# Kernel optimization log

Hardware: AMD Instinct MI355X
Metric: run time of the kernel (lower is better)

## Reference

```python
import jax, jax.numpy as jnp
import numpy as np
import math

B, T, H, NH, L = 8, 1024, 192, 2, 6
FFN, K, VOCAB, OUT, WIN = 768, 3, 256, 192, 4
KC = H // NH  # per-head channels


def _get_rel(emb, t):
    pad = max(t - (WIN + 1), 0)
    start = max(WIN + 1 - t, 0)
    p = jnp.pad(emb, ((pad, pad), (0, 0)))
    return p[start:start + 2 * t - 1]


def _rel_to_abs(x):
    # [b,h,l,2l-1] -> [b,h,l,l]
    b, h, l, _ = x.shape
    x = jnp.pad(x, ((0, 0), (0, 0), (0, 0), (0, 1)))
    xf = x.reshape(b, h, l * 2 * l)
    xf = jnp.pad(xf, ((0, 0), (0, 0), (0, l - 1)))
    return xf.reshape(b, h, l + 1, 2 * l - 1)[:, :, :l, l - 1:]


def _abs_to_rel(x):
    # [b,h,l,l] -> [b,h,l,2l-1]
    b, h, l, _ = x.shape
    x = jnp.pad(x, ((0, 0), (0, 0), (0, 0), (0, l - 1)))
    xf = x.reshape(b, h, l * (2 * l - 1))
    xf = jnp.pad(xf, ((0, 0), (0, 0), (l, 0)))
    return xf.reshape(b, h, l, 2 * l)[:, :, :, 1:]


def _ln(x, g, b):
    # channels-first LayerNorm over axis 1, x: [B,C,T]
    m = jnp.mean(x, 1, keepdims=True)
    v = jnp.var(x, 1, keepdims=True)
    return (x - m) * jax.lax.rsqrt(v + 1e-5) * g[:, None] + b[:, None]


def _conv1d(x, w, b):
    y = jax.lax.conv_general_dilated(x, w, (1,), 'SAME', dimension_numbers=('NCH', 'OIH', 'NCH'))
    return y + b[:, None]


def _attn(x, attn_mask, qw, qb, kw, kb, vw, vb, ow, ob, rel_k, rel_v):
    b, d, t = x.shape
    def proj(w, bb):
        y = jnp.einsum('oc,bct->bot', w, x) + bb[:, None]
        return y.reshape(b, NH, KC, t).transpose(0, 1, 3, 2)  # [b,h,t,kc]
    q, k, v = proj(qw, qb), proj(kw, kb), proj(vw, vb)
    qs = q / math.sqrt(KC)
    scores = jnp.einsum('bhtk,bhsk->bhts', qs, k)
    scores = scores + _rel_to_abs(jnp.einsum('bhtk,mk->bhtm', qs, _get_rel(rel_k, t)))
    scores = jnp.where(attn_mask == 0, -1e4, scores)
    p = jax.nn.softmax(scores, axis=-1)
    o = jnp.einsum('bhts,bhsk->bhtk', p, v)
    o = o + jnp.einsum('bhtm,mk->bhtk', _abs_to_rel(p), _get_rel(rel_v, t))
    o = o.transpose(0, 1, 3, 2).reshape(b, d, t)
    return jnp.einsum('oc,bct->bot', ow, o) + ob[:, None]


def setup_inputs():
    key = jax.random.key(0)
    ks = iter(jax.random.split(key, 40))
    def nrm(shape, scale):
        return jax.random.normal(next(ks), shape, jnp.float32) * scale
    w = 0.05
    inp = {
        'tokens': jax.random.randint(next(ks), (B, T), 0, VOCAB),
        'x_lengths': jax.random.randint(next(ks), (B,), T // 2, T + 1),
        'emb': nrm((VOCAB, H), H ** -0.5),
        'qw': nrm((L, H, H), w), 'qb': jnp.zeros((L, H)),
        'kw': nrm((L, H, H), w), 'kb': jnp.zeros((L, H)),
        'vw': nrm((L, H, H), w), 'vb': jnp.zeros((L, H)),
        'ow': nrm((L, H, H), w), 'ob': jnp.zeros((L, H)),
        'rel_k': nrm((L, 2 * WIN + 1, KC), KC ** -0.5),
        'rel_v': nrm((L, 2 * WIN + 1, KC), KC ** -0.5),
        'ln1_g': jnp.ones((L, H)), 'ln1_b': jnp.zeros((L, H)),
        'f1w': nrm((L, FFN, H, K), w), 'f1b': jnp.zeros((L, FFN)),
        'f2w': nrm((L, H, FFN, K), w), 'f2b': jnp.zeros((L, H)),
        'ln2_g': jnp.ones((L, H)), 'ln2_b': jnp.zeros((L, H)),
        'pw': nrm((2 * OUT, H), w), 'pb': jnp.zeros((2 * OUT,)),
        'eps': jax.random.normal(next(ks), (B, OUT, T), jnp.float32),
    }
    return inp


def reference(tokens, x_lengths, emb, qw, qb, kw, kb, vw, vb, ow, ob, rel_k, rel_v,
              ln1_g, ln1_b, f1w, f1b, f2w, f2b, ln2_g, ln2_b, pw, pb, eps):
    x = emb[tokens].transpose(0, 2, 1) * math.sqrt(H)  # [B,H,T]
    x_mask = (jnp.arange(T) < x_lengths[:, None]).astype(x.dtype)[:, None, :]  # [B,1,T]
    attn_mask = x_mask[:, :, None, :] * x_mask[:, :, :, None]  # [B,1,T,T]
    x = x * x_mask
    for i in range(L):
        y = _attn(x, attn_mask, qw[i], qb[i], kw[i], kb[i], vw[i], vb[i], ow[i], ob[i], rel_k[i], rel_v[i])
        x = _ln(x + y, ln1_g[i], ln1_b[i])
        y = jax.nn.relu(_conv1d(x * x_mask, f1w[i], f1b[i]))
        y = _conv1d(y * x_mask, f2w[i], f2b[i]) * x_mask
        x = _ln(x + y, ln2_g[i], ln2_b[i])
    x = x * x_mask
    stats = (jnp.einsum('oc,bct->bot', pw, x) + pb[:, None]) * x_mask
    m, logs = stats[:, :OUT], stats[:, OUT:]
    z = m + eps * jnp.exp(logs) * x_mask
    return (z, m, logs, x, x_mask)
```

## Files before the change

kernel.cpp:

```cpp
#include <hip/hip_runtime.h>
#include <math.h>

#define BN 8
#define TN 1024
#define HN 192
#define NHN 2
#define KCN 96
#define LN 6
#define FFNN 768
#define OUTN 192
#define QSTR 104
#define M0S 12.0f

typedef short bfrag __attribute__((ext_vector_type(8)));
typedef float f32x4 __attribute__((ext_vector_type(4)));

__device__ __forceinline__ short f2bf(float f) {
    union { float f; unsigned u; } v; v.f = f;
    unsigned r = v.u + 0x7fffu + ((v.u >> 16) & 1u);
    return (short)(r >> 16);
}
__device__ __forceinline__ float bf2f(short s) {
    union { unsigned u; float f; } v;
    v.u = ((unsigned)(unsigned short)s) << 16;
    return v.f;
}
__device__ __forceinline__ int pack2(float a, float b) {
    return (int)(unsigned short)f2bf(a) | (((int)(unsigned short)f2bf(b)) << 16);
}

#define QSCALE 0.10206207261596575f

__global__ void k_cvt(const float* __restrict__ src, short* __restrict__ dst, int n) {
    int i = blockIdx.x * 256 + threadIdx.x;
    if (i < n) dst[i] = f2bf(src[i]);
}
__global__ void k_cvtconv(const float* __restrict__ src, short* __restrict__ dst,
                          int M, int Cin, int n) {
    int i = blockIdx.x * 256 + threadIdx.x;
    if (i >= n) return;
    int tap = i % 3;
    int c = (i / 3) % Cin;
    int m = (i / (3 * Cin)) % M;
    int l = i / (3 * Cin * M);
    dst[(((size_t)l * 3 + tap) * M + m) * Cin + c] = f2bf(src[i]);
}
__global__ void k_cvt_qkv(const float* __restrict__ qw, const float* __restrict__ kw,
                          const float* __restrict__ vw, short* __restrict__ dst, int n) {
    int i = blockIdx.x * 256 + threadIdx.x;
    if (i >= n) return;
    int c = i % 192;
    int r = (i / 192) % 576;
    int l = i / (192 * 576);
    float val, sc = 1.f;
    if (r < 192) { val = qw[((size_t)l * 192 + r) * 192 + c]; sc = QSCALE; }
    else if (r < 384) val = kw[((size_t)l * 192 + (r - 192)) * 192 + c];
    else val = vw[((size_t)l * 192 + (r - 384)) * 192 + c];
    dst[i] = f2bf(val * sc);
}
__global__ void k_cvt_qkvb(const float* __restrict__ qb, const float* __restrict__ kb,
                           const float* __restrict__ vb, float* __restrict__ dst, int n) {
    int i = blockIdx.x * 256 + threadIdx.x;
    if (i >= n) return;
    int r = i % 576;
    int l = i / 576;
    dst[i] = (r < 192) ? qb[l * 192 + r] * QSCALE
           : (r < 384) ? kb[l * 192 + r - 192]
                       : vb[l * 192 + r - 384];
}

__global__ __launch_bounds__(256) void k_embed(const int* __restrict__ tok,
        const int* __restrict__ lens, const float* __restrict__ emb,
        float* __restrict__ x, short* __restrict__ xb) {
    __shared__ float s[HN][65];
    const int b = blockIdx.y, t0 = blockIdx.x * 64, tid = threadIdx.x;
    const int len = lens[b];
    for (int idx = tid; idx < 64 * HN; idx += 256) {
        int tt = idx / HN, c = idx % HN;
        int t = t0 + tt;
        float v = 0.f;
        if (t < len) v = emb[tok[b * TN + t] * HN + c] * 13.856406460551018f;
        s[c][tt] = v;
    }
    __syncthreads();
    for (int idx = tid; idx < 64 * HN; idx += 256) {
        int c = idx >> 6, tt = idx & 63;
        x[((size_t)b * HN + c) * TN + t0 + tt] = s[c][tt];
    }
    for (int idx = tid; idx < 64 * 96; idx += 256) {
        int tt = idx / 96, p = idx % 96;
        ((int*)xb)[((size_t)(b * TN + t0 + tt)) * 96 + p] = pack2(s[2 * p][tt], s[2 * p + 1][tt]);
    }
}

template <int TAPS, bool RELU, bool MASK_OUT, int OUTK, bool KSPLIT2>
__global__ __launch_bounds__(256) void k_mgemm(
        const short* __restrict__ W, const short* __restrict__ X,
        const float* __restrict__ bias, void* __restrict__ Yv,
        float* __restrict__ Yv2,
        const int* __restrict__ lens, int M, int Cin, float oscale) {
    constexpr int P = (TAPS - 1) / 2;
    constexpr int XS = 72;
    __shared__ short Wt[TAPS][64][XS];
    __shared__ short Xt[64 + 2 * P][XS];

    const int b = blockIdx.z;
    const int mtiles = KSPLIT2 ? (gridDim.y >> 1) : gridDim.y;
    const int kg = KSPLIT2 ? (blockIdx.y / mtiles) : 0;
    const int m0 = (KSPLIT2 ? (blockIdx.y % mtiles) : blockIdx.y) * 64;
    const int t0 = blockIdx.x * 64;
    const int len = lens[b];
    const int tid = threadIdx.x;
    const int w = tid >> 6;
    const int lane = tid & 63;
    const int col = lane & 15;
    const int quad = lane >> 4;

    f32x4 acc[4];
#pragma unroll
    for (int st = 0; st < 4; ++st) acc[st] = (f32x4){0.f, 0.f, 0.f, 0.f};

    const int cbeg = KSPLIT2 ? kg * (Cin >> 1) : 0;
    const int cend = KSPLIT2 ? cbeg + (Cin >> 1) : Cin;
    for (int c0 = cbeg; c0 < cend; c0 += 64) {
        __syncthreads();
        for (int i = tid; i < TAPS * 64 * 8; i += 256) {
            int tap = i / (64 * 8);
            int mm = (i / 8) & 63;
            int part = i & 7;
            *(int4*)(&Wt[tap][mm][part * 8]) =
                *(const int4*)(W + ((size_t)tap * M + m0 + mm) * Cin + c0 + part * 8);
        }
        for (int i = tid; i < (64 + 2 * P) * 8; i += 256) {
            int tt = i >> 3;
            int part = i & 7;
            int t = t0 + tt - P;
            int4 v = {0, 0, 0, 0};
            if (t >= 0 && t < TN)
                v = *(const int4*)(X + ((size_t)b * TN + t) * Cin + c0 + part * 8);
            *(int4*)(&Xt[tt][part * 8]) = v;
        }
        __syncthreads();
#pragma unroll
        for (int ks = 0; ks < 2; ++ks) {
#pragma unroll
            for (int tap = 0; tap < TAPS; ++tap) {
                bfrag af = *(const bfrag*)(&Wt[tap][w * 16 + col][ks * 32 + quad * 8]);
#pragma unroll
                for (int st = 0; st < 4; ++st) {
                    bfrag bf = *(const bfrag*)(&Xt[st * 16 + col + tap][ks * 32 + quad * 8]);
                    acc[st] = __builtin_amdgcn_mfma_f32_16x16x32_bf16(af, bf, acc[st], 0, 0, 0);
                }
            }
        }
    }

    const int mbase = m0 + w * 16 + quad * 4;
    float bs[4];
#pragma unroll
    for (int reg = 0; reg < 4; ++reg)
        bs[reg] = (KSPLIT2 && kg) ? 0.f : bias[mbase + reg];
#pragma unroll
    for (int st = 0; st < 4; ++st) {
        int t = t0 + st * 16 + col;
        bool om = MASK_OUT && (t >= len);
        float v[4];
#pragma unroll
        for (int reg = 0; reg < 4; ++reg) {
            float u = (acc[st][reg] + bs[reg]) * oscale;
            if (RELU) u = fmaxf(u, 0.f);
            if (om) u = 0.f;
            v[reg] = u;
        }
        if (OUTK == 0) {
            float* dst = (KSPLIT2 && kg) ? Yv2 : (float*)Yv;
#pragma unroll
            for (int reg = 0; reg < 4; ++reg)
                dst[((size_t)b * M + mbase + reg) * TN + t] = v[reg];
        } else if (OUTK == 1) {
            int2 pk;
            pk.x = pack2(v[0], v[1]);
            pk.y = pack2(v[2], v[3]);
            *(int2*)((short*)Yv + ((size_t)(b * TN + t)) * M + mbase) = pk;
        } else {
#pragma unroll
            for (int reg = 0; reg < 4; ++reg)
                ((short*)Yv)[((size_t)b * M + mbase + reg) * TN + t] = f2bf(v[reg]);
        }
    }
}

__global__ __launch_bounds__(256) void k_qkv(
        const short* __restrict__ W, const short* __restrict__ X,
        const float* __restrict__ bias, short* __restrict__ qo,
        short* __restrict__ ko, short* __restrict__ vo) {
    __shared__ short Wt[64][72];
    __shared__ short Xt[64][72];
    const int b = blockIdx.z;
    const int m0 = blockIdx.y * 64;
    const int t0 = blockIdx.x * 64;
    const int tid = threadIdx.x;
    const int w = tid >> 6;
    const int lane = tid & 63;
    const int col = lane & 15;
    const int quad = lane >> 4;

    f32x4 acc[4];
#pragma unroll
    for (int st = 0; st < 4; ++st) acc[st] = (f32x4){0.f, 0.f, 0.f, 0.f};

    for (int c0 = 0; c0 < 192; c0 += 64) {
        __syncthreads();
        for (int i = tid; i < 512; i += 256) {
            int mm = i >> 3, part = i & 7;
            *(int4*)(&Wt[mm][part * 8]) =
                *(const int4*)(W + ((size_t)(m0 + mm)) * 192 + c0 + part * 8);
        }
        for (int i = tid; i < 512; i += 256) {
            int tt = i >> 3, part = i & 7;
            *(int4*)(&Xt[tt][part * 8]) =
                *(const int4*)(X + ((size_t)(b * TN + t0 + tt)) * 192 + c0 + part * 8);
        }
        __syncthreads();
#pragma unroll
        for (int ks = 0; ks < 2; ++ks) {
            bfrag af = *(const bfrag*)(&Wt[w * 16 + col][ks * 32 + quad * 8]);
#pragma unroll
            for (int st = 0; st < 4; ++st) {
                bfrag bf = *(const bfrag*)(&Xt[st * 16 + col][ks * 32 + quad * 8]);
                acc[st] = __builtin_amdgcn_mfma_f32_16x16x32_bf16(af, bf, acc[st], 0, 0, 0);
            }
        }
    }

    const int mbase = m0 + w * 16 + quad * 4;
    const int proj = m0 / 192;
    const int mloc = mbase - proj * 192;
    float bs[4];
#pragma unroll
    for (int reg = 0; reg < 4; ++reg) bs[reg] = bias[mbase + reg];
#pragma unroll
    for (int st = 0; st < 4; ++st) {
        int t = t0 + st * 16 + col;
        float v[4];
#pragma unroll
        for (int reg = 0; reg < 4; ++reg) v[reg] = acc[st][reg] + bs[reg];
        if (proj < 2) {
            short* dst = (proj == 0) ? qo : ko;
            int2 pk;
            pk.x = pack2(v[0], v[1]);
            pk.y = pack2(v[2], v[3]);
            *(int2*)(dst + ((size_t)(b * TN + t)) * 192 + mloc) = pk;
        } else {
#pragma unroll
            for (int reg = 0; reg < 4; ++reg)
                vo[((size_t)b * 192 + mloc + reg) * TN + t] = f2bf(v[reg]);
        }
    }
}

__global__ __launch_bounds__(512, 4) void k_attn4(
        const short* __restrict__ Q, const short* __restrict__ K,
        const short* __restrict__ V, const float* __restrict__ relk,
        const float* __restrict__ relv, short* __restrict__ accP,
        float* __restrict__ lP, const int* __restrict__ lens) {
    __shared__ short kt[64 * QSTR];
    __shared__ short vt[96 * 72];
    __shared__ short Pt[128 * 72];
    __shared__ short rbt[16 * QSTR];
    __shared__ float rels[128 * 12];
    __shared__ float sband[128 * 12];
    __shared__ float rvs[9 * 96];

    const int b = blockIdx.z;
    const int h = blockIdx.y >> 2, sh = blockIdx.y & 3;
    const int t0 = blockIdx.x * 128;
    const int len = lens[b];
    const int tid = threadIdx.x;
    const int w = tid >> 6;
    const int lane = tid & 63;
    const int col = lane & 15;
    const int quad = lane >> 4;

    const short* Qb = Q + ((size_t)b * TN + t0) * HN + h * KCN;
    const short* Kb = K + ((size_t)b * TN + sh * 256) * HN + h * KCN;
    const short* Vb = V + ((size_t)b * HN + h * KCN) * TN + sh * 256;

    bfrag qf[3];
#pragma unroll
    for (int ks = 0; ks < 3; ++ks)
        qf[ks] = *(const bfrag*)(Qb + (size_t)(w * 16 + col) * HN + ks * 32 + quad * 8);

    for (int i = tid; i < 9 * 96; i += 512) rvs[i] = relv[i];
    for (int i = tid; i < 16 * 96; i += 512) {
        int r = i / 96, c = i % 96;
        rbt[r * QSTR + c] = (r < 9) ? f2bf(relk[r * 96 + c]) : (short)0;
    }
    for (int i = tid; i < 128 * 12; i += 512) sband[i] = -1e30f;
    __syncthreads();

    {
        f32x4 rc = (f32x4){0.f, 0.f, 0.f, 0.f};
#pragma unroll
        for (int ks = 0; ks < 3; ++ks) {
            bfrag bf = *(const bfrag*)(rbt + col * QSTR + ks * 32 + quad * 8);
            rc = __builtin_amdgcn_mfma_f32_16x16x32_bf16(qf[ks], bf, rc, 0, 0, 0);
        }
        if (col < 12) {
#pragma unroll
            for (int reg = 0; reg < 4; ++reg)
                rels[(w * 16 + quad * 4 + reg) * 12 + col] = rc[reg];
        }
    }

    float lsum[4];
    f32x4 accv[6];
#pragma unroll
    for (int r = 0; r < 4; ++r) lsum[r] = 0.f;
#pragma unroll
    for (int n = 0; n < 6; ++n) accv[n] = (f32x4){0.f, 0.f, 0.f, 0.f};

    const int rem = len - sh * 256;
    const int nj = (rem <= 0) ? 0 : ((rem >= 256) ? 4 : ((rem + 63) >> 6));

    for (int j = 0; j < nj; ++j) {
        const int s0g = sh * 256 + j * 64;
        __syncthreads();
        for (int i = tid; i < 768; i += 512) {
            int row = i / 12, part = i % 12;
            *(int4*)(kt + row * QSTR + part * 8) =
                *(const int4*)(Kb + ((size_t)(j * 64 + row)) * HN + part * 8);
        }
        for (int i = tid; i < 768; i += 512) {
            int c = i >> 3, part = i & 7;
            *(int4*)(vt + c * 72 + part * 8) =
                *(const int4*)(Vb + (size_t)c * TN + j * 64 + part * 8);
        }
        __syncthreads();

        f32x4 sacc[4];
#pragma unroll
        for (int st = 0; st < 4; ++st) sacc[st] = (f32x4){0.f, 0.f, 0.f, 0.f};
#pragma unroll
        for (int ks = 0; ks < 3; ++ks) {
#pragma unroll
            for (int st = 0; st < 4; ++st) {
                bfrag bf = *(const bfrag*)(kt + (st * 16 + col) * QSTR + ks * 32 + quad * 8);
                sacc[st] = __builtin_amdgcn_mfma_f32_16x16x32_bf16(qf[ks], bf, sacc[st], 0, 0, 0);
            }
        }

#pragma unroll
        for (int reg = 0; reg < 4; ++reg) {
            const int lq = w * 16 + quad * 4 + reg;
            const int qg = t0 + lq;
#pragma unroll
            for (int st = 0; st < 4; ++st) {
                int sg = s0g + st * 16 + col;
                float v = sacc[st][reg];
                int d = sg - qg + 4;
                bool inb = (d >= 0) && (d <= 8);
                if (inb) v += rels[lq * 12 + d];
                if (sg >= len) v = -1e4f;
                if (inb) sband[lq * 12 + d] = v;
                float p = __expf(v - M0S);
                lsum[reg] += p;
                Pt[lq * 72 + st * 16 + col] = f2bf(p);
            }
        }
#pragma unroll
        for (int ks = 0; ks < 2; ++ks) {
            bfrag af = *(const bfrag*)(Pt + (w * 16 + col) * 72 + ks * 32 + quad * 8);
#pragma unroll
            for (int nt = 0; nt < 6; ++nt) {
                bfrag bf = *(const bfrag*)(vt + (nt * 16 + col) * 72 + ks * 32 + quad * 8);
                accv[nt] = __builtin_amdgcn_mfma_f32_16x16x32_bf16(af, bf, accv[nt], 0, 0, 0);
            }
        }
    }

#pragma unroll
    for (int reg = 0; reg < 4; ++reg) {
        lsum[reg] += __shfl_xor(lsum[reg], 1);
        lsum[reg] += __shfl_xor(lsum[reg], 2);
        lsum[reg] += __shfl_xor(lsum[reg], 4);
        lsum[reg] += __shfl_xor(lsum[reg], 8);
    }
    __syncthreads();

    short* aout = accP + (size_t)sh * BN * TN * HN;
#pragma unroll
    for (int reg = 0; reg < 4; ++reg) {
        const int lq = w * 16 + quad * 4 + reg;
        const int qg = t0 + lq;
        float pb[9];
#pragma unroll
        for (int d = 0; d < 9; ++d)
            pb[d] = __expf(sband[lq * 12 + d] - M0S);
#pragma unroll
        for (int nt = 0; nt < 6; ++nt) {
            int c = nt * 16 + col;
            float r = accv[nt][reg];
#pragma unroll
            for (int d = 0; d < 9; ++d) r += pb[d] * rvs[d * 96 + c];
            aout[((size_t)(b * TN + qg)) * HN + h * KCN + c] = f2bf(r);
        }
        if (col == 0)
            lP[(((size_t)sh * BN + b) * NHN + h) * TN + qg] = lsum[reg];
    }
}

__global__ __launch_bounds__(256) void k_amerge(const short* __restrict__ accP,
        const float* __restrict__ lP, short* __restrict__ O) {
    const int idx = blockIdx.x * 256 + threadIdx.x;
    const int p = idx % 96;
    const int t = (idx / 96) % TN;
    const int b = idx / (96 * TN);
    const int h = p / 48;
    const size_t HS = (size_t)BN * TN * HN / 2;
    float a0 = 0.f, a1 = 0.f, l = 0.f;
#pragma unroll
    for (int sh = 0; sh < 4; ++sh) {
        int v = ((const int*)accP)[HS * sh + idx];
        a0 += bf2f((short)(v & 0xffff));
        a1 += bf2f((short)(v >> 16));
        l += lP[(((size_t)sh * BN + b) * NHN + h) * TN + t];
    }
    float linv = (l > 0.f) ? 1.f / l : 0.f;
    ((int*)O)[idx] = pack2(a0 * linv, a1 * linv);
}

template <bool ADD2>
__global__ __launch_bounds__(256) void k_ln(float* __restrict__ x,
        const float* __restrict__ y, const float* __restrict__ y2,
        const float* __restrict__ g, const float* __restrict__ bb,
        short* __restrict__ xb, const int* __restrict__ lens) {
    __shared__ float s[HN][33];
    __shared__ float red1[256], red2[256];
    __shared__ float mu[32], rs[32];
    const int b = blockIdx.y;
    const int t0 = blockIdx.x * 32;
    const int tid = threadIdx.x;
    const int len = lens[b];

    for (int idx = tid; idx < HN * 32; idx += 256) {
        int c = idx >> 5, tt = idx & 31;
        size_t gi = ((size_t)b * HN + c) * TN + t0 + tt;
        float v = x[gi] + y[gi];
        if (ADD2) v += y2[gi];
        s[c][tt] = v;
    }
    __syncthreads();
    int tt = tid & 31, grp = tid >> 5;
    float sum = 0.f, sum2 = 0.f;
    for (int c = grp * 24; c < grp * 24 + 24; ++c) {
        float v = s[c][tt];
        sum += v;
        sum2 += v * v;
    }
    red1[tid] = sum;
    red2[tid] = sum2;
    __syncthreads();
    if (tid < 32) {
        float tot = 0.f, tot2 = 0.f;
#pragma unroll
        for (int gg = 0; gg < 8; ++gg) { tot += red1[gg * 32 + tid]; tot2 += red2[gg * 32 + tid]; }
        float mean = tot / (float)HN;
        float var = tot2 / (float)HN - mean * mean;
        mu[tid] = mean;
        rs[tid] = rsqrtf(var + 1e-5f);
    }
    __syncthreads();
    for (int idx = tid; idx < HN * 32; idx += 256) {
        int c = idx >> 5, t2 = idx & 31;
        float v = (s[c][t2] - mu[t2]) * rs[t2] * g[c] + bb[c];
        x[((size_t)b * HN + c) * TN + t0 + t2] = v;
    }
    for (int idx = tid; idx < 32 * 96; idx += 256) {
        int t2 = idx / 96, p = idx % 96;
        int c0 = 2 * p;
        float v0 = (s[c0][t2] - mu[t2]) * rs[t2] * g[c0] + bb[c0];
        float v1 = (s[c0 + 1][t2] - mu[t2]) * rs[t2] * g[c0 + 1] + bb[c0 + 1];
        if (t0 + t2 >= len) { v0 = 0.f; v1 = 0.f; }
        ((int*)xb)[((size_t)(b * TN + t0 + t2)) * 96 + p] = pack2(v0, v1);
    }
}

__global__ void k_final(const float* __restrict__ stats, const float* __restrict__ x,
        const float* __restrict__ eps, const int* __restrict__ lens,
        float* __restrict__ out) {
    int idx = blockIdx.x * 256 + threadIdx.x;
    int t = idx % TN;
    int o = (idx / TN) % OUTN;
    int b = idx / (TN * OUTN);
    float maskv = (t < lens[b]) ? 1.f : 0.f;
    const size_t S = (size_t)BN * OUTN * TN;
    float m = stats[((size_t)(b * 2 * OUTN) + o) * TN + t];
    float ls = stats[((size_t)(b * 2 * OUTN) + OUTN + o) * TN + t];
    float e = eps[idx];
    out[idx] = m + e * expf(ls) * maskv;
    out[S + idx] = m;
    out[2 * S + idx] = ls;
    out[3 * S + idx] = x[idx] * maskv;
    if (o == 0) out[4 * S + (size_t)b * TN + t] = maskv;
}

extern "C" void kernel_launch(void* const* d_in, const int* in_sizes, int n_in,
                              void* d_out, int out_size, void* d_ws, size_t ws_size,
                              hipStream_t stream) {
    const int* tok = (const int*)d_in[0];
    const int* lens = (const int*)d_in[1];
    const float* emb = (const float*)d_in[2];
    const float* qw = (const float*)d_in[3];
    const float* qb = (const float*)d_in[4];
    const float* kw = (const float*)d_in[5];
    const float* kb = (const float*)d_in[6];
    const float* vw = (const float*)d_in[7];
    const float* vb = (const float*)d_in[8];
    const float* ow = (const float*)d_in[9];
    const float* ob = (const float*)d_in[10];
    const float* relk = (const float*)d_in[11];
    const float* relv = (const float*)d_in[12];
    const float* ln1g = (const float*)d_in[13];
    const float* ln1b = (const float*)d_in[14];
    const float* f1w = (const float*)d_in[15];
    const float* f1b = (const float*)d_in[16];
    const float* f2w = (const float*)d_in[17];
    const float* f2b = (const float*)d_in[18];
    const float* ln2g = (const float*)d_in[19];
    const float* ln2b = (const float*)d_in[20];
    const float* pw = (const float*)d_in[21];
    const float* pb = (const float*)d_in[22];
    const float* eps = (const float*)d_in[23];

    const size_t BHT = (size_t)BN * HN * TN;
    float* ws = (float*)d_ws;
    float* x = ws;
    float* yf = ws + BHT;
    short* s_xb = (short*)(ws + 2 * BHT);
    short* s_ln = (short*)(ws + 2 * BHT + BHT / 2);
    short* s_q  = (short*)(ws + 3 * BHT);
    short* s_k  = (short*)(ws + 3 * BHT + BHT / 2);
    float* yf2  = ws + 3 * BHT;
    short* s_v  = (short*)(ws + 4 * BHT);
    short* s_o  = (short*)(ws + 4 * BHT + BHT / 2);
    short* accP = (short*)(ws + 5 * BHT);
    short* s_y1 = (short*)(ws + 5 * BHT);
    float* stats = ws + 5 * BHT;
    short* wqkv = (short*)(ws + 7 * BHT);
    short* wo16 = wqkv + (size_t)LN * 3 * HN * HN;
    short* wp16 = wo16 + (size_t)LN * HN * HN;
    short* wf1_16 = wp16 + (size_t)2 * OUTN * HN;
    short* wf2_16 = wf1_16 + (size_t)LN * 3 * FFNN * HN;
    float* bqkv = (float*)(wf2_16 + (size_t)LN * 3 * FFNN * HN);
    float* lP = bqkv + (size_t)LN * 576;

    {
        int nq = LN * 576 * 192;
        k_cvt_qkv<<<dim3((nq + 255) / 256), 256, 0, stream>>>(qw, kw, vw, wqkv, nq);
        int nqb = LN * 576;
        k_cvt_qkvb<<<dim3((nqb + 255) / 256), 256, 0, stream>>>(qb, kb, vb, bqkv, nqb);
        int n1 = LN * HN * HN;
        k_cvt<<<dim3((n1 + 255) / 256), 256, 0, stream>>>(ow, wo16, n1);
        int n2 = 2 * OUTN * HN;
        k_cvt<<<dim3((n2 + 255) / 256), 256, 0, stream>>>(pw, wp16, n2);
        int n3 = LN * FFNN * HN * 3;
        k_cvtconv<<<dim3((n3 + 255) / 256), 256, 0, stream>>>(f1w, wf1_16, FFNN, HN, n3);
        k_cvtconv<<<dim3((n3 + 255) / 256), 256, 0, stream>>>(f2w, wf2_16, HN, FFNN, n3);
    }

    dim3 gemb(TN / 64, BN);
    k_embed<<<gemb, 256, 0, stream>>>(tok, lens, emb, x, s_xb);

    dim3 gproj(TN / 64, HN / 64, BN);
    dim3 gqkv(TN / 64, 9, BN);
    dim3 gf1(TN / 64, FFNN / 64, BN);
    dim3 gf2(TN / 64, 6, BN);
    dim3 gattn(TN / 128, NHN * 4, BN);
    dim3 gmerge((unsigned)(BN * TN * 96 / 256));
    dim3 gln(TN / 32, BN);

    for (int i = 0; i < LN; ++i) {
        const short* qkvwi = wqkv + (size_t)i * 576 * 192;
        const float* qkvbi = bqkv + (size_t)i * 576;
        const short* owi = wo16 + (size_t)i * HN * HN;
        const short* f1wi = wf1_16 + (size_t)i * 3 * FFNN * HN;
        const short* f2wi = wf2_16 + (size_t)i * 3 * FFNN * HN;
        const float* obi = ob + (size_t)i * HN;
        const float* rki = relk + (size_t)i * 9 * KCN;
        const float* rvi = relv + (size_t)i * 9 * KCN;
        const float* l1gi = ln1g + (size_t)i * HN;
        const float* l1bi = ln1b + (size_t)i * HN;
        const float* f1bi = f1b + (size_t)i * FFNN;
        const float* f2bi = f2b + (size_t)i * HN;
        const float* l2gi = ln2g + (size_t)i * HN;
        const float* l2bi = ln2b + (size_t)i * HN;

        k_qkv<<<gqkv, 256, 0, stream>>>(qkvwi, s_xb, qkvbi, s_q, s_k, s_v);
        k_attn4<<<gattn, 512, 0, stream>>>(s_q, s_k, s_v, rki, rvi, accP, lP, lens);
        k_amerge<<<gmerge, 256, 0, stream>>>(accP, lP, s_o);
        k_mgemm<1, false, false, 0, false><<<gproj, 256, 0, stream>>>(owi, s_o, obi, yf, nullptr, lens, HN, HN, 1.f);
        k_ln<false><<<gln, 256, 0, stream>>>(x, yf, nullptr, l1gi, l1bi, s_ln, lens);
        k_mgemm<3, true, true, 1, false><<<gf1, 256, 0, stream>>>(f1wi, s_ln, f1bi, s_y1, nullptr, lens, FFNN, HN, 1.f);
        k_mgemm<3, false, true, 0, true><<<gf2, 256, 0, stream>>>(f2wi, s_y1, f2bi, yf, yf2, lens, HN, FFNN, 1.f);
        k_ln<true><<<gln, 256, 0, stream>>>(x, yf, yf2, l2gi, l2bi, s_xb, lens);
    }

    dim3 gstat(TN / 64, (2 * OUTN) / 64, BN);
    k_mgemm<1, false, true, 0, false><<<gstat, 256, 0, stream>>>(wp16, s_xb, pb, stats, nullptr, lens, 2 * OUTN, HN, 1.f);
    k_final<<<dim3((unsigned)(BHT / 256)), 256, 0, stream>>>(stats, x, eps, lens, (float*)d_out);
}
```

Baseline: 888.4 us.

## Fuse attention merge into output projection and retile GEMMs with full-K staging

Removes the separate attention-merge kernel by folding the four-way partial sum and softmax normalization into the load stage of a new output-projection GEMM that stages the full 192-wide K dimension in shared memory at once. The QKV and stats projections use the same single-pass full-K tiling. The FFN convolutions move to 128-wide time tiles, and the second one uses a three-way K split whose partials are summed in the layer norm. Together these cut kernel launches, intermediate round trips and loop synchronisation, but raise shared-memory use per block and add extra partial-buffer traffic.

```diff
diff --git a/kernel.cpp b/kernel.cpp
--- a/kernel.cpp
+++ b/kernel.cpp
@@ -10,6 +10,7 @@
 #define FFNN 768
 #define OUTN 192
 #define QSTR 104
+#define GSTR 200
 #define M0S 12.0f
 
 typedef short bfrag __attribute__((ext_vector_type(8)));
@@ -93,22 +94,171 @@
     }
 }
 
-template <int TAPS, bool RELU, bool MASK_OUT, int OUTK, bool KSPLIT2>
+template <bool MERGE, bool MASK_OUT>
+__global__ __launch_bounds__(256) void k_g192(
+        const short* __restrict__ W, const short* __restrict__ X,
+        const float* __restrict__ bias, float* __restrict__ Y,
+        const short* __restrict__ accP, const float* __restrict__ lPp,
+        const int* __restrict__ lens, int M) {
+    __shared__ short Wt[64 * GSTR];
+    __shared__ short Xt[64 * GSTR];
+    __shared__ float linv[128];
+    const int b = blockIdx.z, m0 = blockIdx.y * 64, t0 = blockIdx.x * 64;
+    const int len = lens[b];
+    const int tid = threadIdx.x;
+    const int w = tid >> 6, lane = tid & 63, col = lane & 15, quad = lane >> 4;
+
+    if (MERGE) {
+        if (tid < 128) {
+            int tt = tid & 63, h = tid >> 6;
+            float l = 0.f;
+#pragma unroll
+            for (int sh = 0; sh < 4; ++sh)
+                l += lPp[(((size_t)sh * BN + b) * NHN + h) * TN + t0 + tt];
+            linv[tid] = (l > 0.f) ? 1.f / l : 0.f;
+        }
+        __syncthreads();
+    }
+    for (int i = tid; i < 1536; i += 256) {
+        int mm = i / 24, part = i % 24;
+        *(int4*)(Wt + mm * GSTR + part * 8) =
+            *(const int4*)(W + ((size_t)(m0 + mm)) * 192 + part * 8);
+    }
+    for (int i = tid; i < 1536; i += 256) {
+        int tt = i / 24, part = i % 24;
+        if (!MERGE) {
+            *(int4*)(Xt + tt * GSTR + part * 8) =
+                *(const int4*)(X + ((size_t)(b * TN + t0 + tt)) * 192 + part * 8);
+        } else {
+            const size_t base = ((size_t)(b * TN + t0 + tt)) * 192 + part * 8;
+            const size_t HSq = (size_t)BN * TN * HN;
+            float a[8];
+#pragma unroll
+            for (int c = 0; c < 8; ++c) a[c] = 0.f;
+#pragma unroll
+            for (int sh = 0; sh < 4; ++sh) {
+                int4 v = *(const int4*)(accP + sh * HSq + base);
+                const short* sv = (const short*)&v;
+#pragma unroll
+                for (int c = 0; c < 8; ++c) a[c] += bf2f(sv[c]);
+            }
+            float li = linv[(part >= 12 ? 64 : 0) + tt];
+            int4 o;
+            int* oi = (int*)&o;
+#pragma unroll
+            for (int c = 0; c < 4; ++c) oi[c] = pack2(a[2 * c] * li, a[2 * c + 1] * li);
+            *(int4*)(Xt + tt * GSTR + part * 8) = o;
+        }
+    }
+    __syncthreads();
+
+    f32x4 acc[4];
+#pragma unroll
+    for (int st = 0; st < 4; ++st) acc[st] = (f32x4){0.f, 0.f, 0.f, 0.f};
+#pragma unroll
+    for (int ks = 0; ks < 6; ++ks) {
+        bfrag af = *(const bfrag*)(Wt + (w * 16 + col) * GSTR + ks * 32 + quad * 8);
+#pragma unroll
+        for (int st = 0; st < 4; ++st) {
+            bfrag bf = *(const bfrag*)(Xt + (st * 16 + col) * GSTR + ks * 32 + quad * 8);
+            acc[st] = __builtin_amdgcn_mfma_f32_16x16x32_bf16(af, bf, acc[st], 0, 0, 0);
+        }
+    }
+
+    const int mbase = m0 + w * 16 + quad * 4;
+    float bs[4];
+#pragma unroll
+    for (int reg = 0; reg < 4; ++reg) bs[reg] = bias[mbase + reg];
+#pragma unroll
+    for (int st = 0; st < 4; ++st) {
+        int t = t0 + st * 16 + col;
+        bool om = MASK_OUT && (t >= len);
+#pragma unroll
+        for (int reg = 0; reg < 4; ++reg) {
+            float u = acc[st][reg] + bs[reg];
+            if (om) u = 0.f;
+            Y[((size_t)b * M + mbase + reg) * TN + t] = u;
+        }
+    }
+}
+
+__global__ __launch_bounds__(256) void k_qkv2(
+        const short* __restrict__ W, const short* __restrict__ X,
+        const float* __restrict__ bias, short* __restrict__ qo,
+        short* __restrict__ ko, short* __restrict__ vo) {
+    __shared__ short Wt[64 * GSTR];
+    __shared__ short Xt[64 * GSTR];
+    const int b = blockIdx.z, m0 = blockIdx.y * 64, t0 = blockIdx.x * 64;
+    const int tid = threadIdx.x;
+    const int w = tid >> 6, lane = tid & 63, col = lane & 15, quad = lane >> 4;
+
+    for (int i = tid; i < 1536; i += 256) {
+        int mm = i / 24, part = i % 24;
+        *(int4*)(Wt + mm * GSTR + part * 8) =
+            *(const int4*)(W + ((size_t)(m0 + mm)) * 192 + part * 8);
+    }
+    for (int i = tid; i < 1536; i += 256) {
+        int tt = i / 24, part = i % 24;
+        *(int4*)(Xt + tt * GSTR + part * 8) =
+            *(const int4*)(X + ((size_t)(b * TN + t0 + tt)) * 192 + part * 8);
+    }
+    __syncthreads();
+
+    f32x4 acc[4];
+#pragma unroll
+    for (int st = 0; st < 4; ++st) acc[st] = (f32x4){0.f, 0.f, 0.f, 0.f};
+#pragma unroll
+    for (int ks = 0; ks < 6; ++ks) {
+        bfrag af = *(const bfrag*)(Wt + (w * 16 + col) * GSTR + ks * 32 + quad * 8);
+#pragma unroll
+        for (int st = 0; st < 4; ++st) {
+            bfrag bf = *(const bfrag*)(Xt + (st * 16 + col) * GSTR + ks * 32 + quad * 8);
+            acc[st] = __builtin_amdgcn_mfma_f32_16x16x32_bf16(af, bf, acc[st], 0, 0, 0);
+        }
+    }
+
+    const int mbase = m0 + w * 16 + quad * 4;
+    const int proj = m0 / 192;
+    const int mloc = mbase - proj * 192;
+    float bs[4];
+#pragma unroll
+    for (int reg = 0; reg < 4; ++reg) bs[reg] = bias[mbase + reg];
+#pragma unroll
+    for (int st = 0; st < 4; ++st) {
+        int t = t0 + st * 16 + col;
+        float v[4];
+#pragma unroll
+        for (int reg = 0; reg < 4; ++reg) v[reg] = acc[st][reg] + bs[reg];
+        if (proj < 2) {
+            short* dst = (proj == 0) ? qo : ko;
+            int2 pk;
+            pk.x = pack2(v[0], v[1]);
+            pk.y = pack2(v[2], v[3]);
+            *(int2*)(dst + ((size_t)(b * TN + t)) * 192 + mloc) = pk;
+        } else {
+#pragma unroll
+            for (int reg = 0; reg < 4; ++reg)
+                vo[((size_t)b * 192 + mloc + reg) * TN + t] = f2bf(v[reg]);
+        }
+    }
+}
+
+template <int TAPS, int TT, bool RELU, bool MASK_OUT, int OUTK, int KSPLIT>
 __global__ __launch_bounds__(256) void k_mgemm(
         const short* __restrict__ W, const short* __restrict__ X,
         const float* __restrict__ bias, void* __restrict__ Yv,
-        float* __restrict__ Yv2,
-        const int* __restrict__ lens, int M, int Cin, float oscale) {
+        float* __restrict__ Yv2, float* __restrict__ Yv3,
+        const int* __restrict__ lens, int M, int Cin) {
     constexpr int P = (TAPS - 1) / 2;
-    constexpr int XS = 72;
-    __shared__ short Wt[TAPS][64][XS];
-    __shared__ short Xt[64 + 2 * P][XS];
+    constexpr int NST = TT / 16;
+    __shared__ short Wt[TAPS][64][72];
+    __shared__ short Xt[TT + 2 * P][72];
 
     const int b = blockIdx.z;
-    const int mtiles = KSPLIT2 ? (gridDim.y >> 1) : gridDim.y;
-    const int kg = KSPLIT2 ? (blockIdx.y / mtiles) : 0;
-    const int m0 = (KSPLIT2 ? (blockIdx.y % mtiles) : blockIdx.y) * 64;
-    const int t0 = blockIdx.x * 64;
+    const int mtiles = gridDim.y / KSPLIT;
+    const int kg = blockIdx.y / mtiles;
+    const int m0 = (blockIdx.y % mtiles) * 64;
+    const int t0 = blockIdx.x * TT;
     const int len = lens[b];
     const int tid = threadIdx.x;
     const int w = tid >> 6;
@@ -116,12 +266,13 @@
     const int col = lane & 15;
     const int quad = lane >> 4;
 
-    f32x4 acc[4];
-#pragma unroll
-    for (int st = 0; st < 4; ++st) acc[st] = (f32x4){0.f, 0.f, 0.f, 0.f};
-
-    const int cbeg = KSPLIT2 ? kg * (Cin >> 1) : 0;
-    const int cend = KSPLIT2 ? cbeg + (Cin >> 1) : Cin;
+    f32x4 acc[NST];
+#pragma unroll
+    for (int st = 0; st < NST; ++st) acc[st] = (f32x4){0.f, 0.f, 0.f, 0.f};
+
+    const int cspan = Cin / KSPLIT;
+    const int cbeg = kg * cspan;
+    const int cend = cbeg + cspan;
     for (int c0 = cbeg; c0 < cend; c0 += 64) {
         __syncthreads();
         for (int i = tid; i < TAPS * 64 * 8; i += 256) {
@@ -131,7 +282,7 @@
             *(int4*)(&Wt[tap][mm][part * 8]) =
                 *(const int4*)(W + ((size_t)tap * M + m0 + mm) * Cin + c0 + part * 8);
         }
-        for (int i = tid; i < (64 + 2 * P) * 8; i += 256) {
+        for (int i = tid; i < (TT + 2 * P) * 8; i += 256) {
             int tt = i >> 3;
             int part = i & 7;
             int t = t0 + tt - P;
@@ -147,7 +298,7 @@
             for (int tap = 0; tap < TAPS; ++tap) {
                 bfrag af = *(const bfrag*)(&Wt[tap][w * 16 + col][ks * 32 + quad * 8]);
 #pragma unroll
-                for (int st = 0; st < 4; ++st) {
+                for (int st = 0; st < NST; ++st) {
                     bfrag bf = *(const bfrag*)(&Xt[st * 16 + col + tap][ks * 32 + quad * 8]);
                     acc[st] = __builtin_amdgcn_mfma_f32_16x16x32_bf16(af, bf, acc[st], 0, 0, 0);
                 }
@@ -159,102 +310,30 @@
     float bs[4];
 #pragma unroll
     for (int reg = 0; reg < 4; ++reg)
-        bs[reg] = (KSPLIT2 && kg) ? 0.f : bias[mbase + reg];
-#pragma unroll
-    for (int st = 0; st < 4; ++st) {
+        bs[reg] = (KSPLIT > 1 && kg) ? 0.f : bias[mbase + reg];
+#pragma unroll
+    for (int st = 0; st < NST; ++st) {
         int t = t0 + st * 16 + col;
         bool om = MASK_OUT && (t >= len);
         float v[4];
 #pragma unroll
         for (int reg = 0; reg < 4; ++reg) {
-            float u = (acc[st][reg] + bs[reg]) * oscale;
+            float u = acc[st][reg] + bs[reg];
             if (RELU) u = fmaxf(u, 0.f);
             if (om) u = 0.f;
             v[reg] = u;
         }
         if (OUTK == 0) {
-            float* dst = (KSPLIT2 && kg) ? Yv2 : (float*)Yv;
+            float* dst = (KSPLIT > 1) ? (kg == 0 ? (float*)Yv : (kg == 1 ? Yv2 : Yv3))
+                                      : (float*)Yv;
 #pragma unroll
             for (int reg = 0; reg < 4; ++reg)
                 dst[((size_t)b * M + mbase + reg) * TN + t] = v[reg];
-        } else if (OUTK == 1) {
+        } else {
             int2 pk;
             pk.x = pack2(v[0], v[1]);
             pk.y = pack2(v[2], v[3]);
             *(int2*)((short*)Yv + ((size_t)(b * TN + t)) * M + mbase) = pk;
-        } else {
-#pragma unroll
-            for (int reg = 0; reg < 4; ++reg)
-                ((short*)Yv)[((size_t)b * M + mbase + reg) * TN + t] = f2bf(v[reg]);
-        }
-    }
-}
-
-__global__ __launch_bounds__(256) void k_qkv(
-        const short* __restrict__ W, const short* __restrict__ X,
-        const float* __restrict__ bias, short* __restrict__ qo,
-        short* __restrict__ ko, short* __restrict__ vo) {
-    __shared__ short Wt[64][72];
-    __shared__ short Xt[64][72];
-    const int b = blockIdx.z;
-    const int m0 = blockIdx.y * 64;
-    const int t0 = blockIdx.x * 64;
-    const int tid = threadIdx.x;
-    const int w = tid >> 6;
-    const int lane = tid & 63;
-    const int col = lane & 15;
-    const int quad = lane >> 4;
-
-    f32x4 acc[4];
-#pragma unroll
-    for (int st = 0; st < 4; ++st) acc[st] = (f32x4){0.f, 0.f, 0.f, 0.f};
-
-    for (int c0 = 0; c0 < 192; c0 += 64) {
-        __syncthreads();
-        for (int i = tid; i < 512; i += 256) {
-            int mm = i >> 3, part = i & 7;
-            *(int4*)(&Wt[mm][part * 8]) =
-                *(const int4*)(W + ((size_t)(m0 + mm)) * 192 + c0 + part * 8);
-        }
-        for (int i = tid; i < 512; i += 256) {
-            int tt = i >> 3, part = i & 7;
-            *(int4*)(&Xt[tt][part * 8]) =
-                *(const int4*)(X + ((size_t)(b * TN + t0 + tt)) * 192 + c0 + part * 8);
-        }
-        __syncthreads();
-#pragma unroll
-        for (int ks = 0; ks < 2; ++ks) {
-            bfrag af = *(const bfrag*)(&Wt[w * 16 + col][ks * 32 + quad * 8]);
-#pragma unroll
-            for (int st = 0; st < 4; ++st) {
-                bfrag bf = *(const bfrag*)(&Xt[st * 16 + col][ks * 32 + quad * 8]);
-                acc[st] = __builtin_amdgcn_mfma_f32_16x16x32_bf16(af, bf, acc[st], 0, 0, 0);
-            }
-        }
-    }
-
-    const int mbase = m0 + w * 16 + quad * 4;
-    const int proj = m0 / 192;
-    const int mloc = mbase - proj * 192;
-    float bs[4];
-#pragma unroll
-    for (int reg = 0; reg < 4; ++reg) bs[reg] = bias[mbase + reg];
-#pragma unroll
-    for (int st = 0; st < 4; ++st) {
-        int t = t0 + st * 16 + col;
-        float v[4];
-#pragma unroll
-        for (int reg = 0; reg < 4; ++reg) v[reg] = acc[st][reg] + bs[reg];
-        if (proj < 2) {
-            short* dst = (proj == 0) ? qo : ko;
-            int2 pk;
-            pk.x = pack2(v[0], v[1]);
-            pk.y = pack2(v[2], v[3]);
-            *(int2*)(dst + ((size_t)(b * TN + t)) * 192 + mloc) = pk;
-        } else {
-#pragma unroll
-            for (int reg = 0; reg < 4; ++reg)
-                vo[((size_t)b * 192 + mloc + reg) * TN + t] = f2bf(v[reg]);
         }
     }
 }
@@ -410,31 +489,12 @@
     }
 }
 
-__global__ __launch_bounds__(256) void k_amerge(const short* __restrict__ accP,
-        const float* __restrict__ lP, short* __restrict__ O) {
-    const int idx = blockIdx.x * 256 + threadIdx.x;
-    const int p = idx % 96;
-    const int t = (idx / 96) % TN;
-    const int b = idx / (96 * TN);
-    const int h = p / 48;
-    const size_t HS = (size_t)BN * TN * HN / 2;
-    float a0 = 0.f, a1 = 0.f, l = 0.f;
-#pragma unroll
-    for (int sh = 0; sh < 4; ++sh) {
-        int v = ((const int*)accP)[HS * sh + idx];
-        a0 += bf2f((short)(v & 0xffff));
-        a1 += bf2f((short)(v >> 16));
-        l += lP[(((size_t)sh * BN + b) * NHN + h) * TN + t];
-    }
-    float linv = (l > 0.f) ? 1.f / l : 0.f;
-    ((int*)O)[idx] = pack2(a0 * linv, a1 * linv);
-}
-
-template <bool ADD2>
+template <int NADD>
 __global__ __launch_bounds__(256) void k_ln(float* __restrict__ x,
         const float* __restrict__ y, const float* __restrict__ y2,
-        const float* __restrict__ g, const float* __restrict__ bb,
-        short* __restrict__ xb, const int* __restrict__ lens) {
+        const float* __restrict__ y3, const float* __restrict__ g,
+        const float* __restrict__ bb, short* __restrict__ xb,
+        const int* __restrict__ lens) {
     __shared__ float s[HN][33];
     __shared__ float red1[256], red2[256];
     __shared__ float mu[32], rs[32];
@@ -447,7 +507,8 @@
         int c = idx >> 5, tt = idx & 31;
         size_t gi = ((size_t)b * HN + c) * TN + t0 + tt;
         float v = x[gi] + y[gi];
-        if (ADD2) v += y2[gi];
+        if (NADD >= 2) v += y2[gi];
+        if (NADD >= 3) v += y3[gi];
         s[c][tt] = v;
     }
     __syncthreads();
@@ -541,9 +602,9 @@
     short* s_ln = (short*)(ws + 2 * BHT + BHT / 2);
     short* s_q  = (short*)(ws + 3 * BHT);
     short* s_k  = (short*)(ws + 3 * BHT + BHT / 2);
-    float* yf2  = ws + 3 * BHT;
     short* s_v  = (short*)(ws + 4 * BHT);
-    short* s_o  = (short*)(ws + 4 * BHT + BHT / 2);
+    float* p1   = ws + 3 * BHT;
+    float* p2   = ws + 4 * BHT;
     short* accP = (short*)(ws + 5 * BHT);
     short* s_y1 = (short*)(ws + 5 * BHT);
     float* stats = ws + 5 * BHT;
@@ -572,12 +633,11 @@
     dim3 gemb(TN / 64, BN);
     k_embed<<<gemb, 256, 0, stream>>>(tok, lens, emb, x, s_xb);
 
-    dim3 gproj(TN / 64, HN / 64, BN);
     dim3 gqkv(TN / 64, 9, BN);
-    dim3 gf1(TN / 64, FFNN / 64, BN);
-    dim3 gf2(TN / 64, 6, BN);
     dim3 gattn(TN / 128, NHN * 4, BN);
-    dim3 gmerge((unsigned)(BN * TN * 96 / 256));
+    dim3 goproj(TN / 64, HN / 64, BN);
+    dim3 gf1(TN / 128, FFNN / 64, BN);
+    dim3 gf2(TN / 128, 9, BN);
     dim3 gln(TN / 32, BN);
 
     for (int i = 0; i < LN; ++i) {
@@ -596,17 +656,16 @@
         const float* l2gi = ln2g + (size_t)i * HN;
         const float* l2bi = ln2b + (size_t)i * HN;
 
-        k_qkv<<<gqkv, 256, 0, stream>>>(qkvwi, s_xb, qkvbi, s_q, s_k, s_v);
+        k_qkv2<<<gqkv, 256, 0, stream>>>(qkvwi, s_xb, qkvbi, s_q, s_k, s_v);
         k_attn4<<<gattn, 512, 0, stream>>>(s_q, s_k, s_v, rki, rvi, accP, lP, lens);
-        k_amerge<<<gmerge, 256, 0, stream>>>(accP, lP, s_o);
-        k_mgemm<1, false, false, 0, false><<<gproj, 256, 0, stream>>>(owi, s_o, obi, yf, nullptr, lens, HN, HN, 1.f);
-        k_ln<false><<<gln, 256, 0, stream>>>(x, yf, nullptr, l1gi, l1bi, s_ln, lens);
-        k_mgemm<3, true, true, 1, false><<<gf1, 256, 0, stream>>>(f1wi, s_ln, f1bi, s_y1, nullptr, lens, FFNN, HN, 1.f);
-        k_mgemm<3, false, true, 0, true><<<gf2, 256, 0, stream>>>(f2wi, s_y1, f2bi, yf, yf2, lens, HN, FFNN, 1.f);
-        k_ln<true><<<gln, 256, 0, stream>>>(x, yf, yf2, l2gi, l2bi, s_xb, lens);
+        k_g192<true, false><<<goproj, 256, 0, stream>>>(owi, nullptr, obi, yf, accP, lP, lens, HN);
+        k_ln<1><<<gln, 256, 0, stream>>>(x, yf, nullptr, nullptr, l1gi, l1bi, s_ln, lens);
+        k_mgemm<3, 128, true, true, 1, 1><<<gf1, 256, 0, stream>>>(f1wi, s_ln, f1bi, s_y1, nullptr, nullptr, lens, FFNN, HN);
+        k_mgemm<3, 128, false, true, 0, 3><<<gf2, 256, 0, stream>>>(f2wi, s_y1, f2bi, yf, p1, p2, lens, HN, FFNN);
+        k_ln<3><<<gln, 256, 0, stream>>>(x, yf, p1, p2, l2gi, l2bi, s_xb, lens);
     }
 
     dim3 gstat(TN / 64, (2 * OUTN) / 64, BN);
-    k_mgemm<1, false, true, 0, false><<<gstat, 256, 0, stream>>>(wp16, s_xb, pb, stats, nullptr, lens, 2 * OUTN, HN, 1.f);
+    k_g192<false, true><<<gstat, 256, 0, stream>>>(wp16, s_xb, pb, stats, nullptr, nullptr, lens, 2 * OUTN);
     k_final<<<dim3((unsigned)(BHT / 256)), 256, 0, stream>>>(stats, x, eps, lens, (float*)d_out);
 }
```

New measurement: 880.1 us. Within noise of the previous version (-0.9%).
